# Performance work log

Hardware: AMD Instinct MI355X
Metric: run time of the kernel (lower is better)

Reference implementation:

```python
import jax, jax.numpy as jnp
import numpy as np

N_NODES = 100000
N_EDGES = 3200000
IN_FEAT = 128
HIDDEN = 128
CLASSES = 32


def gcn_conv(x, edge_index, W, b, n_nodes):
    """PyG GCNConv: linear -> symmetric-normalized scatter-add with self-loops -> +bias."""
    src, dst = edge_index[0], edge_index[1]
    loop = jnp.arange(n_nodes, dtype=edge_index.dtype)
    src = jnp.concatenate([src, loop])
    dst = jnp.concatenate([dst, loop])
    # degree (with self-loops) on destination nodes
    deg = jax.ops.segment_sum(jnp.ones_like(dst, dtype=x.dtype), dst, num_segments=n_nodes)
    dinv = jnp.where(deg > 0, jax.lax.rsqrt(deg), 0.0)
    norm = dinv[src] * dinv[dst]  # [E+N]
    h = x @ W  # [N, out]
    msg = h[src] * norm[:, None]  # gather + scale, [E+N, out]
    out = jax.ops.segment_sum(msg, dst, num_segments=n_nodes)  # scatter-add
    return out + b


def setup_inputs() -> dict:
    key = jax.random.key(0)
    k1, k2, k3, k4 = jax.random.split(key, 4)
    x = jax.random.normal(k1, (N_NODES, IN_FEAT), dtype=jnp.float32)
    edge_index = jax.random.randint(k2, (2, N_EDGES), 0, N_NODES, dtype=jnp.int64)
    W1 = jax.random.normal(k3, (IN_FEAT, HIDDEN), dtype=jnp.float32) / np.sqrt(IN_FEAT)
    b1 = jnp.zeros((HIDDEN,), dtype=jnp.float32)
    W2 = jax.random.normal(k4, (HIDDEN, CLASSES), dtype=jnp.float32) / np.sqrt(HIDDEN)
    b2 = jnp.zeros((CLASSES,), dtype=jnp.float32)
    return {"x": x, "edge_index": edge_index, "W1": W1, "b1": b1, "W2": W2, "b2": b2}


def reference(x, edge_index, W1, b1, W2, b2):
    n = x.shape[0]
    h = gcn_conv(x, edge_index, W1, b1, n)
    h = jax.nn.relu(h)
    # dropout p=0.5 is identity in eval mode
    out = gcn_conv(h, edge_index, W2, b2, n)
    return out
```

## Files before the change

kernel.cpp:

```cpp
#include <hip/hip_runtime.h>

#define N_NODES 100000
#define N_EDGES 3200000
#define F_IN 128
#define F_HID 128
#define F_OUT 32
#define CAP 96

#define NBUCK 391
#define CAPB 8960
#define EPT 32

#define BM 64
#define BK 16
#define XPAD 68

typedef float f32x2 __attribute__((ext_vector_type(2)));

__device__ inline unsigned pack_bf16(float a, float b) {
    unsigned ua = __float_as_uint(a);
    ua = (ua + 0x7fffu + ((ua >> 16) & 1u)) >> 16;
    unsigned ub = __float_as_uint(b);
    ub = (ub + 0x7fffu + ((ub >> 16) & 1u)) >> 16;
    return ua | (ub << 16);
}
__device__ inline float lo16(unsigned u) { return __uint_as_float(u << 16); }
__device__ inline float hi16(unsigned u) { return __uint_as_float(u & 0xffff0000u); }

__global__ __launch_bounds__(256) void k_part(const int* __restrict__ ei,
                                              int* __restrict__ gcur,
                                              unsigned long long* __restrict__ stage) {
    __shared__ int cnt[NBUCK];
    __shared__ int base[NBUCK];
    int tid = threadIdx.x;
    for (int i = tid; i < NBUCK; i += 256) cnt[i] = 0;
    __syncthreads();

    long e0 = (long)blockIdx.x * (256 * EPT);
#pragma unroll 4
    for (int i = 0; i < EPT; ++i) {
        long e = e0 + i * 256 + tid;
        if (e < N_EDGES) atomicAdd(&cnt[ei[N_EDGES + e] >> 8], 1);
    }
    __syncthreads();
    for (int i = tid; i < NBUCK; i += 256) {
        base[i] = atomicAdd(&gcur[i], cnt[i]);
        cnt[i] = 0;
    }
    __syncthreads();
#pragma unroll 4
    for (int i = 0; i < EPT; ++i) {
        long e = e0 + i * 256 + tid;
        if (e < N_EDGES) {
            int s = ei[e];
            int d = ei[N_EDGES + e];
            int b = d >> 8;
            int pos = base[b] + atomicAdd(&cnt[b], 1);
            if (pos < CAPB)
                stage[(size_t)b * CAPB + pos] = ((unsigned long long)(unsigned)d << 32) | (unsigned)s;
        }
    }
}

__global__ __launch_bounds__(256) void k_csr(const unsigned long long* __restrict__ stage,
                                             const int* __restrict__ gcur,
                                             int* __restrict__ csr,
                                             int* __restrict__ deg,
                                             float* __restrict__ dinv) {
    __shared__ int cnt[256];
    int b = blockIdx.x;
    int tid = threadIdx.x;
    cnt[tid] = 0;
    __syncthreads();

    int d0 = b << 8;
    int m = gcur[b];
    if (m > CAPB) m = CAPB;
    const unsigned long long* sp = stage + (size_t)b * CAPB;
    for (int i = tid; i < m; i += 256) {
        unsigned long long rec = __builtin_nontemporal_load(sp + i);
        int s = (int)(unsigned)rec;
        int d = (int)(rec >> 32);
        int pos = atomicAdd(&cnt[d - d0], 1);
        if (pos < CAP) csr[(size_t)d * CAP + pos] = s;
    }
    __syncthreads();
    int dd = d0 + tid;
    if (dd < N_NODES) {
        int dg = cnt[tid];
        deg[dd] = dg;
        dinv[dd] = rsqrtf((float)(dg + 1));
    }
}

__global__ __launch_bounds__(256) void k_gemm1(const float* __restrict__ x,
                                               const float* __restrict__ W1,
                                               const float* __restrict__ dinv,
                                               unsigned* __restrict__ g1u) {
    __shared__ float xT[BK][XPAD];
    __shared__ float wt[BK][F_HID];

    int tid = threadIdx.x;
    int m0 = blockIdx.x * BM;

    int rg = tid >> 4;
    int cg = tid & 15;
    int r0 = rg * 4;
    int c0 = cg * 8;

    int lr = tid >> 2;
    int lk = (tid & 3) * 4;
    int gr = m0 + lr;
    int grc = gr < N_NODES ? gr : N_NODES - 1;
    const float* xrow = x + (size_t)grc * F_IN + lk;

    float acc[4][8];
#pragma unroll
    for (int i = 0; i < 4; ++i)
#pragma unroll
        for (int j = 0; j < 8; ++j) acc[i][j] = 0.f;

    for (int k0 = 0; k0 < F_IN; k0 += BK) {
        float4 v = *(const float4*)(xrow + k0);
        const float4* w4 = (const float4*)(W1 + (size_t)k0 * F_HID);
        float4 wv0 = w4[tid];
        float4 wv1 = w4[tid + 256];

        xT[lk + 0][lr] = v.x;
        xT[lk + 1][lr] = v.y;
        xT[lk + 2][lr] = v.z;
        xT[lk + 3][lr] = v.w;
        ((float4*)wt)[tid] = wv0;
        ((float4*)wt)[tid + 256] = wv1;
        __syncthreads();

#pragma unroll
        for (int k = 0; k < BK; ++k) {
            float a[4], b[8];
            *(float4*)a = *(const float4*)&xT[k][r0];
            *(float4*)(b + 0) = *(const float4*)&wt[k][c0];
            *(float4*)(b + 4) = *(const float4*)&wt[k][c0 + 4];
#pragma unroll
            for (int i = 0; i < 4; ++i)
#pragma unroll
                for (int j = 0; j < 8; ++j)
                    acc[i][j] = fmaf(a[i], b[j], acc[i][j]);
        }
        __syncthreads();
    }

#pragma unroll
    for (int i = 0; i < 4; ++i) {
        int n = m0 + r0 + i;
        if (n < N_NODES) {
            float s = dinv[n];
            uint4 o;
            o.x = pack_bf16(acc[i][0] * s, acc[i][1] * s);
            o.y = pack_bf16(acc[i][2] * s, acc[i][3] * s);
            o.z = pack_bf16(acc[i][4] * s, acc[i][5] * s);
            o.w = pack_bf16(acc[i][6] * s, acc[i][7] * s);
            *(uint4*)(g1u + (size_t)n * 64 + (c0 >> 1)) = o;
        }
    }
}

__global__ __launch_bounds__(256) void k_pull1_gemm2(const int* __restrict__ csr,
                                                     const int* __restrict__ deg_i,
                                                     const unsigned* __restrict__ g1u,
                                                     const float* __restrict__ dinv,
                                                     const float* __restrict__ b1,
                                                     const float* __restrict__ W2,
                                                     unsigned* __restrict__ g2u) {
    __shared__ float w2l[F_HID * F_OUT];
    __shared__ float al[4][F_HID];
    {
        const float4* w4 = (const float4*)W2;
        float4* wl4 = (float4*)w2l;
#pragma unroll
        for (int i = 0; i < 4; ++i)
            wl4[threadIdx.x + i * 256] = w4[threadIdx.x + i * 256];
    }
    int lane = threadIdx.x & 63;
    int wv = threadIdx.x >> 6;
    int n = blockIdx.x * 4 + wv;

    unsigned u0 = g1u[(size_t)n * 64 + lane];
    float a0x = lo16(u0), a0y = hi16(u0);
    float a1x = 0.f, a1y = 0.f, a2x = 0.f, a2y = 0.f, a3x = 0.f, a3y = 0.f;
    int deg = deg_i[n];
    if (deg > CAP) deg = CAP;
    const int* crow = csr + (size_t)n * CAP;
    for (int e0 = 0; e0 < deg; e0 += 64) {
        int rem = deg - e0;
        int m = rem < 64 ? rem : 64;
        int sidx = (lane < m) ? __builtin_nontemporal_load(crow + e0 + lane) : 0;
        int j = 0;
        for (; j + 3 < m; j += 4) {
            int s0 = __shfl(sidx, j);
            int s1 = __shfl(sidx, j + 1);
            int s2 = __shfl(sidx, j + 2);
            int s3 = __shfl(sidx, j + 3);
            unsigned v0 = g1u[(size_t)s0 * 64 + lane];
            unsigned v1 = g1u[(size_t)s1 * 64 + lane];
            unsigned v2 = g1u[(size_t)s2 * 64 + lane];
            unsigned v3 = g1u[(size_t)s3 * 64 + lane];
            a0x += lo16(v0); a0y += hi16(v0);
            a1x += lo16(v1); a1y += hi16(v1);
            a2x += lo16(v2); a2y += hi16(v2);
            a3x += lo16(v3); a3y += hi16(v3);
        }
        for (; j < m; ++j) {
            int s0 = __shfl(sidx, j);
            unsigned v0 = g1u[(size_t)s0 * 64 + lane];
            a0x += lo16(v0); a0y += hi16(v0);
        }
    }
    float ax = (a0x + a1x) + (a2x + a3x);
    float ay = (a0y + a1y) + (a2y + a3y);

    float di = dinv[n];
    float2 bb = *(const float2*)(b1 + lane * 2);
    float a0 = fmaxf(fmaf(di, ax, bb.x), 0.f);
    float a1 = fmaxf(fmaf(di, ay, bb.y), 0.f);
    *(float2*)(&al[wv][lane * 2]) = make_float2(a0, a1);
    __syncthreads();

    int j = lane & 31, kh = lane >> 5;
    float sum = 0.f;
#pragma unroll
    for (int kk = 0; kk < 64; ++kk) {
        int k = kh * 64 + kk;
        sum = fmaf(al[wv][k], w2l[k * F_OUT + j], sum);
    }
    sum += __shfl_xor(sum, 32);
    float sv = sum * di;
    int fl16 = lane & 15;
    float sa = __shfl(sv, fl16 * 2);
    float sb = __shfl(sv, fl16 * 2 + 1);
    if (lane < 16) g2u[(size_t)n * 16 + fl16] = pack_bf16(sa, sb);
}

__global__ __launch_bounds__(256) void k_pull2(const int* __restrict__ csr,
                                               const int* __restrict__ deg_i,
                                               const unsigned* __restrict__ g2u,
                                               const float* __restrict__ dinv,
                                               const float* __restrict__ b2,
                                               float* __restrict__ out) {
    int lane = threadIdx.x & 63;
    int wv = threadIdx.x >> 6;
    int qw = lane >> 4, fl = lane & 15;
    int n = blockIdx.x * 16 + wv * 4 + qw;

    unsigned u0 = g2u[(size_t)n * 16 + fl];
    float a0x = lo16(u0), a0y = hi16(u0);
    float a1x = 0.f, a1y = 0.f, a2x = 0.f, a2y = 0.f, a3x = 0.f, a3y = 0.f;
    int deg = deg_i[n];
    if (deg > CAP) deg = CAP;
    const int* crow = csr + (size_t)n * CAP;
    for (int e0 = 0; e0 < deg; e0 += 16) {
        int rem = deg - e0;
        int m = rem < 16 ? rem : 16;
        int sidx = (fl < m) ? __builtin_nontemporal_load(crow + e0 + fl) : 0;
        int j = 0;
        for (; j + 3 < m; j += 4) {
            int s0 = __shfl(sidx, j, 16);
            int s1 = __shfl(sidx, j + 1, 16);
            int s2 = __shfl(sidx, j + 2, 16);
            int s3 = __shfl(sidx, j + 3, 16);
            unsigned v0 = g2u[(size_t)s0 * 16 + fl];
            unsigned v1 = g2u[(size_t)s1 * 16 + fl];
            unsigned v2 = g2u[(size_t)s2 * 16 + fl];
            unsigned v3 = g2u[(size_t)s3 * 16 + fl];
            a0x += lo16(v0); a0y += hi16(v0);
            a1x += lo16(v1); a1y += hi16(v1);
            a2x += lo16(v2); a2y += hi16(v2);
            a3x += lo16(v3); a3y += hi16(v3);
        }
        for (; j < m; ++j) {
            int s0 = __shfl(sidx, j, 16);
            unsigned v0 = g2u[(size_t)s0 * 16 + fl];
            a0x += lo16(v0); a0y += hi16(v0);
        }
    }
    float ax = (a0x + a1x) + (a2x + a3x);
    float ay = (a0y + a1y) + (a2y + a3y);

    float di = dinv[n];
    float2 bb = *(const float2*)(b2 + fl * 2);
    f32x2 o;
    o.x = fmaf(di, ax, bb.x);
    o.y = fmaf(di, ay, bb.y);
    __builtin_nontemporal_store(o, (f32x2*)(out + (size_t)n * F_OUT + fl * 2));
}

extern "C" void kernel_launch(void* const* d_in, const int* in_sizes, int n_in,
                              void* d_out, int out_size, void* d_ws, size_t ws_size,
                              hipStream_t stream) {
    const float* x  = (const float*)d_in[0];
    const int*   ei = (const int*)d_in[1];
    const float* W1 = (const float*)d_in[2];
    const float* b1 = (const float*)d_in[3];
    const float* W2 = (const float*)d_in[4];
    const float* b2 = (const float*)d_in[5];
    float* out = (float*)d_out;

    char* ws = (char*)d_ws;
    int*      deg   = (int*)(ws);
    float*    dinv  = (float*)(ws + 524288);
    int*      gcur  = (int*)(ws + 1048576);
    int*      csr   = (int*)(ws + 1572864);
    unsigned long long* stage = (unsigned long long*)(ws + 40000000);
    unsigned* g1u   = (unsigned*)(ws + 68028416);
    unsigned* g2u   = (unsigned*)(ws + 93628416);

    (void)hipMemsetAsync(gcur, 0, 4096, stream);
    k_part<<<(N_EDGES + 256 * EPT - 1) / (256 * EPT), 256, 0, stream>>>(ei, gcur, stage);
    k_csr<<<NBUCK, 256, 0, stream>>>(stage, gcur, csr, deg, dinv);

    k_gemm1<<<(N_NODES + BM - 1) / BM, 256, 0, stream>>>(x, W1, dinv, g1u);

    k_pull1_gemm2<<<N_NODES / 4, 256, 0, stream>>>(csr, deg, g1u, dinv, b1, W2, g2u);
    k_pull2<<<N_NODES / 16, 256, 0, stream>>>(csr, deg, g2u, dinv, b2, out);
}
```

Baseline: 301.3 us.

## Pack staged edges into 32 bits and restructure both pull kernels' gathers

The partition staging record shrinks from 64 to 32 bits: the local destination goes in the upper bits and the source in the low 17 bits. This halves staging traffic between k_part and k_csr. The layer-1 pull now reads its CSR indices up front into two registers and takes neighbor ids with scalar readlane instead of shuffles. The layer-2 pull moves from 4 nodes per wave to 1 node per wave, with 4 edge groups of 16 lanes each and a final cross-lane reduction. That gives more memory parallelism per node at the cost of 4x more waves and idle lanes for low-degree nodes.

```diff
diff --git a/kernel.cpp b/kernel.cpp
--- a/kernel.cpp
+++ b/kernel.cpp
@@ -29,7 +29,7 @@
 
 __global__ __launch_bounds__(256) void k_part(const int* __restrict__ ei,
                                               int* __restrict__ gcur,
-                                              unsigned long long* __restrict__ stage) {
+                                              unsigned* __restrict__ stage) {
     __shared__ int cnt[NBUCK];
     __shared__ int base[NBUCK];
     int tid = threadIdx.x;
@@ -57,12 +57,12 @@
             int b = d >> 8;
             int pos = base[b] + atomicAdd(&cnt[b], 1);
             if (pos < CAPB)
-                stage[(size_t)b * CAPB + pos] = ((unsigned long long)(unsigned)d << 32) | (unsigned)s;
+                stage[(size_t)b * CAPB + pos] = ((unsigned)(d & 255) << 17) | (unsigned)s;
         }
     }
 }
 
-__global__ __launch_bounds__(256) void k_csr(const unsigned long long* __restrict__ stage,
+__global__ __launch_bounds__(256) void k_csr(const unsigned* __restrict__ stage,
                                              const int* __restrict__ gcur,
                                              int* __restrict__ csr,
                                              int* __restrict__ deg,
@@ -76,13 +76,13 @@
     int d0 = b << 8;
     int m = gcur[b];
     if (m > CAPB) m = CAPB;
-    const unsigned long long* sp = stage + (size_t)b * CAPB;
+    const unsigned* sp = stage + (size_t)b * CAPB;
     for (int i = tid; i < m; i += 256) {
-        unsigned long long rec = __builtin_nontemporal_load(sp + i);
-        int s = (int)(unsigned)rec;
-        int d = (int)(rec >> 32);
-        int pos = atomicAdd(&cnt[d - d0], 1);
-        if (pos < CAP) csr[(size_t)d * CAP + pos] = s;
+        unsigned rec = __builtin_nontemporal_load(sp + i);
+        int s = (int)(rec & 0x1ffffu);
+        int dl = (int)(rec >> 17);
+        int pos = atomicAdd(&cnt[dl], 1);
+        if (pos < CAP) csr[(size_t)(d0 + dl) * CAP + pos] = s;
     }
     __syncthreads();
     int dd = d0 + tid;
@@ -182,55 +182,70 @@
     }
     int lane = threadIdx.x & 63;
     int wv = threadIdx.x >> 6;
-    int n = blockIdx.x * 4 + wv;
-
-    unsigned u0 = g1u[(size_t)n * 64 + lane];
-    float a0x = lo16(u0), a0y = hi16(u0);
-    float a1x = 0.f, a1y = 0.f, a2x = 0.f, a2y = 0.f, a3x = 0.f, a3y = 0.f;
+    int n = __builtin_amdgcn_readfirstlane(blockIdx.x * 4 + wv);
+
     int deg = deg_i[n];
     if (deg > CAP) deg = CAP;
     const int* crow = csr + (size_t)n * CAP;
-    for (int e0 = 0; e0 < deg; e0 += 64) {
-        int rem = deg - e0;
-        int m = rem < 64 ? rem : 64;
-        int sidx = (lane < m) ? __builtin_nontemporal_load(crow + e0 + lane) : 0;
-        int j = 0;
-        for (; j + 3 < m; j += 4) {
-            int s0 = __shfl(sidx, j);
-            int s1 = __shfl(sidx, j + 1);
-            int s2 = __shfl(sidx, j + 2);
-            int s3 = __shfl(sidx, j + 3);
-            unsigned v0 = g1u[(size_t)s0 * 64 + lane];
-            unsigned v1 = g1u[(size_t)s1 * 64 + lane];
-            unsigned v2 = g1u[(size_t)s2 * 64 + lane];
-            unsigned v3 = g1u[(size_t)s3 * 64 + lane];
-            a0x += lo16(v0); a0y += hi16(v0);
-            a1x += lo16(v1); a1y += hi16(v1);
-            a2x += lo16(v2); a2y += hi16(v2);
-            a3x += lo16(v3); a3y += hi16(v3);
-        }
-        for (; j < m; ++j) {
-            int s0 = __shfl(sidx, j);
-            unsigned v0 = g1u[(size_t)s0 * 64 + lane];
-            a0x += lo16(v0); a0y += hi16(v0);
-        }
-    }
-    float ax = (a0x + a1x) + (a2x + a3x);
-    float ay = (a0y + a1y) + (a2y + a3y);
+    int sidx0 = __builtin_nontemporal_load(crow + lane);
+    int sidx1 = __builtin_nontemporal_load(crow + 64 + (lane & 31));
+
+    f32x2 ac0, ac1, ac2, ac3;
+    {
+        unsigned us = g1u[(size_t)n * 64 + lane];
+        ac0 = (f32x2){lo16(us), hi16(us)};
+        ac1 = (f32x2){0.f, 0.f}; ac2 = ac1; ac3 = ac1;
+    }
+
+#define GATHER(S, ACC)                                            \
+    {                                                             \
+        const unsigned* p = g1u + ((size_t)(unsigned)(S) << 6);   \
+        unsigned v = p[lane];                                     \
+        ACC += (f32x2){lo16(v), hi16(v)};                         \
+    }
+
+    int m1 = deg < 64 ? deg : 64;
+    int j = 0;
+    for (; j + 3 < m1; j += 4) {
+        int s0 = __builtin_amdgcn_readlane(sidx0, j);
+        int s1 = __builtin_amdgcn_readlane(sidx0, j + 1);
+        int s2 = __builtin_amdgcn_readlane(sidx0, j + 2);
+        int s3 = __builtin_amdgcn_readlane(sidx0, j + 3);
+        GATHER(s0, ac0) GATHER(s1, ac1) GATHER(s2, ac2) GATHER(s3, ac3)
+    }
+    for (; j < m1; ++j) {
+        int s0 = __builtin_amdgcn_readlane(sidx0, j);
+        GATHER(s0, ac0)
+    }
+    int m2 = deg - 64;
+    for (j = 0; j + 3 < m2; j += 4) {
+        int s0 = __builtin_amdgcn_readlane(sidx1, j);
+        int s1 = __builtin_amdgcn_readlane(sidx1, j + 1);
+        int s2 = __builtin_amdgcn_readlane(sidx1, j + 2);
+        int s3 = __builtin_amdgcn_readlane(sidx1, j + 3);
+        GATHER(s0, ac0) GATHER(s1, ac1) GATHER(s2, ac2) GATHER(s3, ac3)
+    }
+    for (; j < m2; ++j) {
+        int s0 = __builtin_amdgcn_readlane(sidx1, j);
+        GATHER(s0, ac0)
+    }
+#undef GATHER
+
+    f32x2 a = (ac0 + ac1) + (ac2 + ac3);
 
     float di = dinv[n];
     float2 bb = *(const float2*)(b1 + lane * 2);
-    float a0 = fmaxf(fmaf(di, ax, bb.x), 0.f);
-    float a1 = fmaxf(fmaf(di, ay, bb.y), 0.f);
+    float a0 = fmaxf(fmaf(di, a.x, bb.x), 0.f);
+    float a1 = fmaxf(fmaf(di, a.y, bb.y), 0.f);
     *(float2*)(&al[wv][lane * 2]) = make_float2(a0, a1);
     __syncthreads();
 
-    int j = lane & 31, kh = lane >> 5;
+    int jj = lane & 31, kh = lane >> 5;
     float sum = 0.f;
 #pragma unroll
     for (int kk = 0; kk < 64; ++kk) {
         int k = kh * 64 + kk;
-        sum = fmaf(al[wv][k], w2l[k * F_OUT + j], sum);
+        sum = fmaf(al[wv][k], w2l[k * F_OUT + jj], sum);
     }
     sum += __shfl_xor(sum, 32);
     float sv = sum * di;
@@ -248,49 +263,39 @@
                                                float* __restrict__ out) {
     int lane = threadIdx.x & 63;
     int wv = threadIdx.x >> 6;
-    int qw = lane >> 4, fl = lane & 15;
-    int n = blockIdx.x * 16 + wv * 4 + qw;
-
-    unsigned u0 = g2u[(size_t)n * 16 + fl];
-    float a0x = lo16(u0), a0y = hi16(u0);
-    float a1x = 0.f, a1y = 0.f, a2x = 0.f, a2y = 0.f, a3x = 0.f, a3y = 0.f;
+    int n = __builtin_amdgcn_readfirstlane(blockIdx.x * 4 + wv);
+    int fl = lane & 15, eq = lane >> 4;
+
     int deg = deg_i[n];
     if (deg > CAP) deg = CAP;
     const int* crow = csr + (size_t)n * CAP;
-    for (int e0 = 0; e0 < deg; e0 += 16) {
-        int rem = deg - e0;
-        int m = rem < 16 ? rem : 16;
-        int sidx = (fl < m) ? __builtin_nontemporal_load(crow + e0 + fl) : 0;
-        int j = 0;
-        for (; j + 3 < m; j += 4) {
-            int s0 = __shfl(sidx, j, 16);
-            int s1 = __shfl(sidx, j + 1, 16);
-            int s2 = __shfl(sidx, j + 2, 16);
-            int s3 = __shfl(sidx, j + 3, 16);
-            unsigned v0 = g2u[(size_t)s0 * 16 + fl];
-            unsigned v1 = g2u[(size_t)s1 * 16 + fl];
-            unsigned v2 = g2u[(size_t)s2 * 16 + fl];
-            unsigned v3 = g2u[(size_t)s3 * 16 + fl];
-            a0x += lo16(v0); a0y += hi16(v0);
-            a1x += lo16(v1); a1y += hi16(v1);
-            a2x += lo16(v2); a2y += hi16(v2);
-            a3x += lo16(v3); a3y += hi16(v3);
-        }
-        for (; j < m; ++j) {
-            int s0 = __shfl(sidx, j, 16);
-            unsigned v0 = g2u[(size_t)s0 * 16 + fl];
-            a0x += lo16(v0); a0y += hi16(v0);
-        }
-    }
-    float ax = (a0x + a1x) + (a2x + a3x);
-    float ay = (a0y + a1y) + (a2y + a3y);
-
-    float di = dinv[n];
-    float2 bb = *(const float2*)(b2 + fl * 2);
-    f32x2 o;
-    o.x = fmaf(di, ax, bb.x);
-    o.y = fmaf(di, ay, bb.y);
-    __builtin_nontemporal_store(o, (f32x2*)(out + (size_t)n * F_OUT + fl * 2));
+
+    f32x2 acc = {0.f, 0.f}, acc2 = {0.f, 0.f};
+    for (int e0 = 0; e0 < deg; e0 += 8) {
+        int ip0 = e0 + eq, ip1 = e0 + 4 + eq;
+        bool ok0 = ip0 < deg, ok1 = ip1 < deg;
+        int s0 = ok0 ? __builtin_nontemporal_load(crow + ip0) : 0;
+        int s1 = ok1 ? __builtin_nontemporal_load(crow + ip1) : 0;
+        unsigned v0 = ok0 ? g2u[(unsigned)s0 * 16u + fl] : 0u;
+        unsigned v1 = ok1 ? g2u[(unsigned)s1 * 16u + fl] : 0u;
+        acc += (f32x2){lo16(v0), hi16(v0)};
+        acc2 += (f32x2){lo16(v1), hi16(v1)};
+    }
+    acc += acc2;
+    acc.x += __shfl_xor(acc.x, 32);
+    acc.y += __shfl_xor(acc.y, 32);
+    acc.x += __shfl_xor(acc.x, 16);
+    acc.y += __shfl_xor(acc.y, 16);
+
+    if (eq == 0) {
+        unsigned us = g2u[(size_t)n * 16 + fl];
+        float di = dinv[n];
+        float2 bb = *(const float2*)(b2 + fl * 2);
+        f32x2 o;
+        o.x = fmaf(di, acc.x + lo16(us), bb.x);
+        o.y = fmaf(di, acc.y + hi16(us), bb.y);
+        __builtin_nontemporal_store(o, (f32x2*)(out + (size_t)n * F_OUT + fl * 2));
+    }
 }
 
 extern "C" void kernel_launch(void* const* d_in, const int* in_sizes, int n_in,
@@ -309,9 +314,9 @@
     float*    dinv  = (float*)(ws + 524288);
     int*      gcur  = (int*)(ws + 1048576);
     int*      csr   = (int*)(ws + 1572864);
-    unsigned long long* stage = (unsigned long long*)(ws + 40000000);
-    unsigned* g1u   = (unsigned*)(ws + 68028416);
-    unsigned* g2u   = (unsigned*)(ws + 93628416);
+    unsigned* stage = (unsigned*)(ws + 40000000);
+    unsigned* g1u   = (unsigned*)(ws + 54016000);
+    unsigned* g2u   = (unsigned*)(ws + 79616000);
 
     (void)hipMemsetAsync(gcur, 0, 4096, stream);
     k_part<<<(N_EDGES + 256 * EPT - 1) / (256 * EPT), 256, 0, stream>>>(ei, gcur, stage);
@@ -320,5 +325,5 @@
     k_gemm1<<<(N_NODES + BM - 1) / BM, 256, 0, stream>>>(x, W1, dinv, g1u);
 
     k_pull1_gemm2<<<N_NODES / 4, 256, 0, stream>>>(csr, deg, g1u, dinv, b1, W2, g2u);
-    k_pull2<<<N_NODES / 16, 256, 0, stream>>>(csr, deg, g2u, dinv, b2, out);
-}
+    k_pull2<<<N_NODES / 4, 256, 0, stream>>>(csr, deg, g2u, dinv, b2, out);
+}
```

Result: slower. 341.0 us (+13.2%).
